# Kernel tuning notes

Measured on AMD Instinct MI355X. Metric: run time of the kernel, lower is better.

## Reference

```python
import math
import jax, jax.numpy as jnp
import numpy as np
from jax import lax

CELL_SIZE = 8
N_BINS = 9
SIGNED = False


def _conv3x3(x, k):
    # x: [N,1,H,W], k: [1,1,3,3]; padding=1 (SAME), stride 1
    return lax.conv_general_dilated(
        x, k, window_strides=(1, 1), padding=[(1, 1), (1, 1)],
        dimension_numbers=("NCHW", "OIHW", "NCHW"))


def setup_inputs() -> dict:
    key = jax.random.key(0)
    x = jax.random.uniform(key, (64, 1, 512, 512), dtype=jnp.float32)
    sobel_x = jnp.array([[-1., 0., 1.], [-2., 0., 2.], [-1., 0., 1.]],
                        dtype=jnp.float32).reshape(1, 1, 3, 3)
    sobel_y = jnp.array([[-1., -2., -1.], [0., 0., 0.], [1., 2., 1.]],
                        dtype=jnp.float32).reshape(1, 1, 3, 3)
    return {"x": x, "sobel_x": sobel_x, "sobel_y": sobel_y}


def reference(x, sobel_x, sobel_y):
    n, _, H, W = x.shape
    angle_range = 2 * math.pi if SIGNED else math.pi

    gx = _conv3x3(x, sobel_x)  # [N,1,H,W]
    gy = _conv3x3(x, sobel_y)
    mag = jnp.sqrt(gx * gx + gy * gy)          # [N,1,H,W]
    ang = jnp.arctan2(gx, gy)                  # note: atan2(gx, gy) as in source
    ang = ang + math.pi if SIGNED else jnp.abs(ang)
    bins = jnp.floor(ang / angle_range * (N_BINS - 1)).astype(jnp.int32)  # [N,1,H,W]

    # scatter_(dim=1): one-hot write of magnitudes into bin channel
    onehot = jax.nn.one_hot(bins[:, 0], N_BINS, axis=1, dtype=mag.dtype)  # [N,nb,H,W]
    out = onehot * mag                                                     # [N,nb,H,W]

    # AvgPool2d(cell,stride=cell) * cell**2 == sum over each cell
    cs = CELL_SIZE
    hog = out.reshape(n, N_BINS, H // cs, cs, W // cs, cs).sum(axis=(3, 5))
    return hog.reshape(-1)
```

## Files before the change

kernel.cpp:

```cpp
#include <hip/hip_runtime.h>
#include <math.h>

#define IMG_H 512
#define IMG_W 512
#define NB 9

__global__ __launch_bounds__(256, 4) void hog_kernel(const float* __restrict__ x,
                                                     float* __restrict__ out) {
#pragma clang fp contract(off)
    const int tid  = threadIdx.x;
    const int w    = tid >> 6;
    const int lane = tid & 63;
    const int cl   = lane & 31;
    const int half = lane >> 5;

    const int cx = ((w & 1) << 5) | cl;
    const int cy = (blockIdx.x << 1) | (w >> 1);
    const int n  = blockIdx.y;

    const float* img = x + (size_t)n * (IMG_H * IMG_W);
    const int x0 = cx << 3;
    const int y0 = (cy << 3) + (half << 2);

    float a[10], b[10], c[10];
    float acc[NB];
#pragma unroll
    for (int k = 0; k < NB; ++k) acc[k] = 0.0f;

    auto load_row = [&](float* r, int y) {
        if (y < 0 || y >= IMG_H) {
#pragma unroll
            for (int i = 0; i < 10; ++i) r[i] = 0.0f;
            return;
        }
        const float* row = img + (size_t)y * IMG_W;
        const float4 p0 = *(const float4*)(row + x0);
        const float4 p1 = *(const float4*)(row + x0 + 4);
        r[1] = p0.x; r[2] = p0.y; r[3] = p0.z; r[4] = p0.w;
        r[5] = p1.x; r[6] = p1.y; r[7] = p1.z; r[8] = p1.w;
        r[0] = (x0 == 0)         ? 0.0f : row[x0 - 1];
        r[9] = (x0 + 8 >= IMG_W) ? 0.0f : row[x0 + 8];
    };

    load_row(a, y0 - 1);
    load_row(b, y0);

    const float PI_F = 3.14159274101257324f;
    const float T1F  = 0.41421356237309503f;
    const float T3F  = 2.41421356237309503f;
    const float KPI  = 2.54647909f;
    const float EPS  = 5e-5f;

#pragma unroll
    for (int ry = 0; ry < 4; ++ry) {
        load_row(c, y0 + ry + 1);

#pragma unroll
        for (int j = 0; j < 8; ++j) {
            const float A0 = a[j], A1 = a[j + 1], A2 = a[j + 2];
            const float B0 = b[j], B2 = b[j + 2];
            const float C0 = c[j], C1 = c[j + 1], C2 = c[j + 2];

            const float gx = ((-A0 + (A2 - 2.0f * B0)) + (2.0f * B2 - C0)) + C2;
            const float gy = (((-A0 - 2.0f * A1) + (-A2)) + (C0 + 2.0f * C1)) + C2;

            const float u = fabsf(gx);
            const float W = fabsf(gy);
            const float q = u * u + W * W;
            const float mag = sqrtf(q);

            const float b1 = W * T1F;
            const float b3 = W * T3F;
            const int cnt = (int)(u > b1) + (int)(u > b3) + (int)(u > W);
            int bin = (gy > 0.0f) ? cnt : 7 - cnt;
            float wA = mag;

            const float KW = KPI * W;
            const float E  = EPS * q;
            const float md = fminf(fminf(fabsf(u - b1), fabsf(u - b3)),
                                   fminf(fabsf(u - W), u));

            if (md * KW < E) {
                const float angf = (float)atan2((double)u, (double)gy);
                const float tc = (float)((double)angf / (double)PI_F) * 8.0f;
                int bc = (int)tc;
                bin = bc > 8 ? 8 : bc;
                const float tn = roundf(tc);
                const int B = (int)tn;
                if (B >= 1 && B <= 8 && fabsf(tc - tn) < 4e-6f &&
                    mag <= 1.05f) {
                    const float hw = 0.5f * mag;
                    bin = B - 1; wA = hw;
#pragma unroll
                    for (int k = 0; k < NB; ++k)
                        acc[k] += (k == B) ? hw : 0.0f;
                }
                if (bin == 8) {
                    acc[8] += wA;
                    wA = 0.0f; bin = 0;
                }
            }

#pragma unroll
            for (int k = 0; k < 8; ++k)
                acc[k] += (bin == k) ? wA : 0.0f;
        }

#pragma unroll
        for (int i = 0; i < 10; ++i) { a[i] = b[i]; b[i] = c[i]; }
    }

#pragma unroll
    for (int k = 0; k < NB; ++k)
        acc[k] += __shfl_xor(acc[k], 32, 64);

    float* o = out + (size_t)n * (NB * 64 * 64) + (size_t)cy * 64 + cx;
    if (half == 0) {
#pragma unroll
        for (int k = 0; k < 5; ++k) o[(size_t)k * 4096] = acc[k];
    } else {
#pragma unroll
        for (int k = 5; k < NB; ++k) o[(size_t)k * 4096] = acc[k];
    }
}

extern "C" void kernel_launch(void* const* d_in, const int* in_sizes, int n_in,
                              void* d_out, int out_size, void* d_ws, size_t ws_size,
                              hipStream_t stream) {
    const float* x = (const float*)d_in[0];
    float* out = (float*)d_out;
    hog_kernel<<<dim3(32, 64, 1), dim3(256, 1, 1), 0, stream>>>(x, out);
}
```

Before: 119.4 us.

## Split each HOG cell across four threads and use branchless sign-split bin accumulation

Each 8x8 cell is now handled by four lanes, each covering a 4x4 quadrant, so the grid doubles and every thread does half as much serial work. Partial histograms are combined with two xor shuffles. The per-pixel one-hot over 8 bins is replaced by a branchless scheme: thresholds are turned into masked differences across two 4-entry accumulators split by the sign of gy. The aim is fewer selects per pixel and more parallelism, at the cost of more redundant halo loads and extra shuffle work.

```diff
diff --git a/kernel.cpp b/kernel.cpp
--- a/kernel.cpp
+++ b/kernel.cpp
@@ -11,39 +11,39 @@
     const int tid  = threadIdx.x;
     const int w    = tid >> 6;
     const int lane = tid & 63;
-    const int cl   = lane & 31;
-    const int half = lane >> 5;
+    const int cl   = lane & 15;
+    const int qid  = lane >> 4;
+    const int sr   = qid >> 1;
+    const int sc   = qid & 1;
 
-    const int cx = ((w & 1) << 5) | cl;
-    const int cy = (blockIdx.x << 1) | (w >> 1);
+    const int cx = (w << 4) | cl;
+    const int cy = blockIdx.x;
     const int n  = blockIdx.y;
 
     const float* img = x + (size_t)n * (IMG_H * IMG_W);
-    const int x0 = cx << 3;
-    const int y0 = (cy << 3) + (half << 2);
+    const int x0 = (cx << 3) + (sc << 2);
+    const int y0 = (cy << 3) + (sr << 2);
 
-    float a[10], b[10], c[10];
-    float acc[NB];
+    float r[6][6];
 #pragma unroll
-    for (int k = 0; k < NB; ++k) acc[k] = 0.0f;
-
-    auto load_row = [&](float* r, int y) {
+    for (int i = 0; i < 6; ++i) {
+        const int y = y0 - 1 + i;
         if (y < 0 || y >= IMG_H) {
 #pragma unroll
-            for (int i = 0; i < 10; ++i) r[i] = 0.0f;
-            return;
+            for (int j = 0; j < 6; ++j) r[i][j] = 0.0f;
+        } else {
+            const float* row = img + (size_t)y * IMG_W;
+            const float4 p = *(const float4*)(row + x0);
+            r[i][1] = p.x; r[i][2] = p.y; r[i][3] = p.z; r[i][4] = p.w;
+            r[i][0] = (x0 == 0)           ? 0.0f : row[x0 - 1];
+            r[i][5] = (x0 + 4 >= IMG_W)   ? 0.0f : row[x0 + 4];
         }
-        const float* row = img + (size_t)y * IMG_W;
-        const float4 p0 = *(const float4*)(row + x0);
-        const float4 p1 = *(const float4*)(row + x0 + 4);
-        r[1] = p0.x; r[2] = p0.y; r[3] = p0.z; r[4] = p0.w;
-        r[5] = p1.x; r[6] = p1.y; r[7] = p1.z; r[8] = p1.w;
-        r[0] = (x0 == 0)         ? 0.0f : row[x0 - 1];
-        r[9] = (x0 + 8 >= IMG_W) ? 0.0f : row[x0 + 8];
-    };
+    }
 
-    load_row(a, y0 - 1);
-    load_row(b, y0);
+    float accA[4], accB[4], acc8;
+#pragma unroll
+    for (int k = 0; k < 4; ++k) { accA[k] = 0.0f; accB[k] = 0.0f; }
+    acc8 = 0.0f;
 
     const float PI_F = 3.14159274101257324f;
     const float T1F  = 0.41421356237309503f;
@@ -53,13 +53,11 @@
 
 #pragma unroll
     for (int ry = 0; ry < 4; ++ry) {
-        load_row(c, y0 + ry + 1);
-
 #pragma unroll
-        for (int j = 0; j < 8; ++j) {
-            const float A0 = a[j], A1 = a[j + 1], A2 = a[j + 2];
-            const float B0 = b[j], B2 = b[j + 2];
-            const float C0 = c[j], C1 = c[j + 1], C2 = c[j + 2];
+        for (int j = 0; j < 4; ++j) {
+            const float A0 = r[ry][j],     A1 = r[ry][j + 1], A2 = r[ry][j + 2];
+            const float B0 = r[ry + 1][j],                    B2 = r[ry + 1][j + 2];
+            const float C0 = r[ry + 2][j], C1 = r[ry + 2][j + 1], C2 = r[ry + 2][j + 2];
 
             const float gx = ((-A0 + (A2 - 2.0f * B0)) + (2.0f * B2 - C0)) + C2;
             const float gy = (((-A0 - 2.0f * A1) + (-A2)) + (C0 + 2.0f * C1)) + C2;
@@ -71,56 +69,75 @@
 
             const float b1 = W * T1F;
             const float b3 = W * T3F;
-            const int cnt = (int)(u > b1) + (int)(u > b3) + (int)(u > W);
-            int bin = (gy > 0.0f) ? cnt : 7 - cnt;
-            float wA = mag;
+            const bool c1 = u > b1;
+            const bool c2 = u > W;
+            const bool c3 = u > b3;
+            const bool s  = gy > 0.0f;
 
             const float KW = KPI * W;
             const float E  = EPS * q;
             const float md = fminf(fminf(fabsf(u - b1), fabsf(u - b3)),
                                    fminf(fabsf(u - W), u));
+            const bool flag = md * KW < E;
 
-            if (md * KW < E) {
+            const float w0 = flag ? 0.0f : mag;
+            const float wP = s ? w0 : 0.0f;
+            const float wN = w0 - wP;
+            const float p1 = c1 ? wP : 0.0f;
+            const float p2 = c2 ? wP : 0.0f;
+            const float p3 = c3 ? wP : 0.0f;
+            const float n1 = c1 ? wN : 0.0f;
+            const float n2 = c2 ? wN : 0.0f;
+            const float n3 = c3 ? wN : 0.0f;
+            accA[0] += wP - p1; accA[1] += p1 - p2;
+            accA[2] += p2 - p3; accA[3] += p3;
+            accB[0] += wN - n1; accB[1] += n1 - n2;
+            accB[2] += n2 - n3; accB[3] += n3;
+
+            if (flag) {
                 const float angf = (float)atan2((double)u, (double)gy);
                 const float tc = (float)((double)angf / (double)PI_F) * 8.0f;
                 int bc = (int)tc;
-                bin = bc > 8 ? 8 : bc;
+                int bin = bc > 8 ? 8 : bc;
+                float wA = mag;
                 const float tn = roundf(tc);
                 const int B = (int)tn;
                 if (B >= 1 && B <= 8 && fabsf(tc - tn) < 4e-6f &&
                     mag <= 1.05f) {
                     const float hw = 0.5f * mag;
+                    accA[0] += (B == 0) ? hw : 0.0f;
+                    accA[1] += (B == 1) ? hw : 0.0f;
+                    accA[2] += (B == 2) ? hw : 0.0f;
+                    accA[3] += (B == 3) ? hw : 0.0f;
+                    accB[3] += (B == 4) ? hw : 0.0f;
+                    accB[2] += (B == 5) ? hw : 0.0f;
+                    accB[1] += (B == 6) ? hw : 0.0f;
+                    accB[0] += (B == 7) ? hw : 0.0f;
+                    acc8    += (B == 8) ? hw : 0.0f;
                     bin = B - 1; wA = hw;
-#pragma unroll
-                    for (int k = 0; k < NB; ++k)
-                        acc[k] += (k == B) ? hw : 0.0f;
                 }
-                if (bin == 8) {
-                    acc[8] += wA;
-                    wA = 0.0f; bin = 0;
-                }
+                accA[0] += (bin == 0) ? wA : 0.0f;
+                accA[1] += (bin == 1) ? wA : 0.0f;
+                accA[2] += (bin == 2) ? wA : 0.0f;
+                accA[3] += (bin == 3) ? wA : 0.0f;
+                accB[3] += (bin == 4) ? wA : 0.0f;
+                accB[2] += (bin == 5) ? wA : 0.0f;
+                accB[1] += (bin == 6) ? wA : 0.0f;
+                accB[0] += (bin == 7) ? wA : 0.0f;
+                acc8    += (bin == 8) ? wA : 0.0f;
             }
-
-#pragma unroll
-            for (int k = 0; k < 8; ++k)
-                acc[k] += (bin == k) ? wA : 0.0f;
         }
-
-#pragma unroll
-        for (int i = 0; i < 10; ++i) { a[i] = b[i]; b[i] = c[i]; }
     }
 
+    const float vals[NB] = {accA[0], accA[1], accA[2], accA[3],
+                            accB[3], accB[2], accB[1], accB[0], acc8};
+    float* o = out + (size_t)n * (NB * 64 * 64) + (size_t)cy * 64 + cx;
 #pragma unroll
-    for (int k = 0; k < NB; ++k)
-        acc[k] += __shfl_xor(acc[k], 32, 64);
-
-    float* o = out + (size_t)n * (NB * 64 * 64) + (size_t)cy * 64 + cx;
-    if (half == 0) {
-#pragma unroll
-        for (int k = 0; k < 5; ++k) o[(size_t)k * 4096] = acc[k];
-    } else {
-#pragma unroll
-        for (int k = 5; k < NB; ++k) o[(size_t)k * 4096] = acc[k];
+    for (int k = 0; k < NB; ++k) {
+        float v = vals[k];
+        v += __shfl_xor(v, 16, 64);
+        v += __shfl_xor(v, 32, 64);
+        if ((k & 3) == qid) o[(size_t)k * 4096] = v;
     }
 }
 
@@ -129,5 +146,5 @@
                               hipStream_t stream) {
     const float* x = (const float*)d_in[0];
     float* out = (float*)d_out;
-    hog_kernel<<<dim3(32, 64, 1), dim3(256, 1, 1), 0, stream>>>(x, out);
+    hog_kernel<<<dim3(64, 64, 1), dim3(256, 1, 1), 0, stream>>>(x, out);
 }
```

After: 119.1 us. About the same (-0.3%).
